# Optimization experiments

Measured on AMD Instinct MI355X. Metric: run time of the kernel, lower is better.

Reference implementation:

```python
import jax, jax.numpy as jnp
import numpy as np

EPS = 1e-5

def rmsnorm(x, w):
    return x * jax.lax.rsqrt(jnp.mean(x * x, axis=-1, keepdims=True) + EPS) * w

def setup_inputs() -> dict:
    key = jax.random.key(0)
    ks = jax.random.split(key, 10)
    b, d, n, k, r, l = 64, 256, 16, 4, 16, 256
    inp = {}
    inp['x_1'] = jax.random.normal(ks[0], (b, d), jnp.float32)
    inp['x_2'] = jax.random.normal(ks[1], (b, d), jnp.float32)
    inp['norm_w'] = jnp.ones((d,), jnp.float32)
    inp['conv_w'] = jax.random.normal(ks[2], (d, 1, k), jnp.float32) * 0.2
    inp['conv_b'] = jax.random.normal(ks[3], (d,), jnp.float32) * 0.02
    inp['in_w'] = jax.random.normal(ks[4], (2 * d, d), jnp.float32) * 0.02
    inp['xproj_w'] = jax.random.normal(ks[5], (r + 2 * n, d), jnp.float32) * 0.02
    inp['dt_w'] = jax.random.normal(ks[6], (d, r), jnp.float32) * 0.02
    inp['dt_b'] = jax.random.normal(ks[7], (d,), jnp.float32) * 0.02
    inp['out_w'] = jax.random.normal(ks[8], (d, d), jnp.float32) * 0.02
    # A = repeat(arange(1, n+1), 'n -> d n'); A_log = log(A)
    inp['A_log'] = jnp.tile(jnp.log(jnp.arange(1, n + 1, dtype=jnp.float32)), (d, 1))
    inp['D'] = jnp.ones((d,), jnp.float32)
    inp['l'] = l
    return inp

def _dwconv(x, conv_w, conv_b, l):
    # x: (b, l, d); depthwise causal-ish conv with padding k-1 on both sides, truncate to l
    d = x.shape[-1]
    k = conv_w.shape[-1]
    xt = x.transpose(0, 2, 1)  # (b, d, l)
    out = jax.lax.conv_general_dilated(
        xt, conv_w, window_strides=(1,), padding=[(k - 1, k - 1)],
        dimension_numbers=('NCH', 'OIH', 'NCH'), feature_group_count=d)
    out = out[:, :, :l] + conv_b[None, :, None]
    return out.transpose(0, 2, 1)  # (b, l, d)

def reference(x_1, x_2, norm_w, conv_w, conv_b, in_w, xproj_w, dt_w, dt_b, out_w, A_log, D, l):
    b, d = x_1.shape
    n = A_log.shape[1]
    r = dt_w.shape[1]
    # RMSNorm then broadcast along sequence
    x1 = jnp.broadcast_to(rmsnorm(x_1, norm_w)[:, None, :], (b, l, d))
    x2 = jnp.broadcast_to(rmsnorm(x_2, norm_w)[:, None, :], (b, l, d))
    # in_proj (no bias), split into x and res
    xr1 = x1 @ in_w.T
    x1c, res1 = xr1[..., :d], xr1[..., d:]
    xr2 = x2 @ in_w.T
    x2c, _ = xr2[..., :d], xr2[..., d:]
    # depthwise conv + silu
    x1s = jax.nn.silu(_dwconv(x1c, conv_w, conv_b, l))
    x2s = jax.nn.silu(_dwconv(x2c, conv_w, conv_b, l))
    # ssm: delta/B/C from x2s, scanned input u = x1s
    A = -jnp.exp(A_log)  # (d, n)
    xdbl = x2s @ xproj_w.T  # (b, l, r + 2n)
    delta, B, C = xdbl[..., :r], xdbl[..., r:r + n], xdbl[..., r + n:]
    delta = jax.nn.softplus(delta @ dt_w.T + dt_b)  # (b, l, d)
    deltaA = jnp.exp(jnp.einsum('bld,dn->bldn', delta, A))  # (b, l, d, n)
    dBu = (delta * x1s)[..., None] * B[:, :, None, :]  # (b, l, d, n)
    def step(h, inputs):
        dA_i, dBu_i, C_i = inputs  # (b,d,n), (b,d,n), (b,n)
        h = dA_i * h + dBu_i
        y = jnp.einsum('bdn,bn->bd', h, C_i)
        return h, y
    h0 = jnp.zeros((b, d, n), x1s.dtype)
    _, ys = jax.lax.scan(step, h0, (deltaA.transpose(1, 0, 2, 3),
                                     dBu.transpose(1, 0, 2, 3),
                                     C.transpose(1, 0, 2)))
    y = ys.transpose(1, 0, 2) + x1s * D  # (b, l, d)
    y = y * jax.nn.silu(res1)
    out = rmsnorm(y @ out_w.T, norm_w)
    return out[:, -1, :]
```

## Files before the change

### kernel.cpp

```cpp
#include <hip/hip_runtime.h>
#include <math.h>

#define D 256
#define N 16
#define R 16

#define WS_X1C  0
#define WS_RES1 16384
#define WS_X2C  32768

__device__ __forceinline__ float silu_f(float x) { return x / (1.0f + expf(-x)); }
__device__ __forceinline__ float softplus_f(float x) {
    return fmaxf(x, 0.0f) + log1pf(expf(-fabsf(x)));
}

__global__ __launch_bounds__(256) void k_inw(
    const float* __restrict__ x1_in, const float* __restrict__ x2_in,
    const float* __restrict__ norm_w, const float* __restrict__ in_w,
    float* __restrict__ ws)
{
    __shared__ float s_n[D];
    __shared__ float s_red[4];
    const int t  = threadIdx.x;
    const int g0 = blockIdx.x * 64;
    const int b  = g0 / 768;
    const int o0 = g0 % 768;
    const bool use2 = (o0 >= 512);
    const int q = t & 3;
    const int o = o0 + (t >> 2);
    const int row = (o >= 512) ? (o - 512) : o;

    const float* __restrict__ wr = in_w + (size_t)row * D;
    float4 w[16];
    #pragma unroll
    for (int k = 0; k < 16; ++k) w[k] = *(const float4*)(wr + q * 4 + 16 * k);

    const float* __restrict__ xrow = (use2 ? x2_in : x1_in) + (size_t)b * D;
    const float v = xrow[t];
    float p = v * v;
    #pragma unroll
    for (int off = 32; off >= 1; off >>= 1) p += __shfl_down(p, off, 64);
    if ((t & 63) == 0) s_red[t >> 6] = p;
    __syncthreads();
    const float ss = s_red[0] + s_red[1] + s_red[2] + s_red[3];
    s_n[t] = v * rsqrtf(ss * (1.0f / D) + 1e-5f) * norm_w[t];
    __syncthreads();

    float acc = 0.0f;
    #pragma unroll
    for (int k = 0; k < 16; ++k) {
        const int e = q * 4 + 16 * k;
        const float4 n4 = *(const float4*)(s_n + e);
        acc += w[k].x*n4.x + w[k].y*n4.y + w[k].z*n4.z + w[k].w*n4.w;
    }
    acc += __shfl_xor(acc, 1, 64);
    acc += __shfl_xor(acc, 2, 64);
    if (q == 0) {
        const int jj = o & 255;
        float* dst = (o < 256) ? (ws + WS_X1C)
                   : (o < 512) ? (ws + WS_RES1)
                               : (ws + WS_X2C);
        dst[b * D + jj] = acc;
    }
}

__global__ __launch_bounds__(1024) void k_fused(
    const float* __restrict__ conv_w, const float* __restrict__ conv_b,
    const float* __restrict__ xproj_w, const float* __restrict__ dt_w,
    const float* __restrict__ dt_b, const float* __restrict__ A_log,
    const float* __restrict__ Dp, const int* __restrict__ l_ptr,
    const float* __restrict__ out_w, const float* __restrict__ norm_w,
    const float* __restrict__ ws, float* __restrict__ out)
{
    __shared__ float s_x2s[4][D];
    __shared__ float s_xdbl[4][48];
    __shared__ float s_y[D];
    __shared__ float s_z[D];
    __shared__ float s_red[4];
    const int b = blockIdx.x;
    const int t = threadIdx.x;
    const int l = *l_ptr;
    const int q   = t & 3;
    const int dot = t >> 2;

    const float* __restrict__ orow = out_w + (size_t)dot * D;
    float4 wo[8];
    #pragma unroll
    for (int k = 0; k < 8; ++k) wo[k] = *(const float4*)(orow + q * 4 + 16 * k);

    float x1c = 0.0f, x2c = 0.0f, res1 = 0.0f, cb = 0.0f, dtb = 0.0f,
          dpj = 0.0f, wnj = 0.0f;
    float4 cw = make_float4(0.f, 0.f, 0.f, 0.f);
    float dtr[R];
    float alog[N];
    if (t < D) {
        x1c  = ws[WS_X1C  + b * D + t];
        x2c  = ws[WS_X2C  + b * D + t];
        res1 = ws[WS_RES1 + b * D + t];
        cw   = *(const float4*)(conv_w + 4 * t);
        cb   = conv_b[t];
        dtb  = dt_b[t];
        dpj  = Dp[t];
        wnj  = norm_w[t];
        const float* __restrict__ dtrow = dt_w + (size_t)t * R;
        #pragma unroll
        for (int qq = 0; qq < R; ++qq) dtr[qq] = dtrow[qq];
        const float* __restrict__ arow = A_log + (size_t)t * N;
        #pragma unroll
        for (int n = 0; n < N; ++n) alog[n] = arow[n];
    }

    float x1s[4];
    if (t < D) {
        float ksum[4];
        ksum[0] = cw.w;
        ksum[1] = cw.z + cw.w;
        ksum[2] = cw.y + cw.z + cw.w;
        ksum[3] = cw.x + cw.y + cw.z + cw.w;
        #pragma unroll
        for (int tc = 0; tc < 4; ++tc) {
            x1s[tc] = silu_f(ksum[tc] * x1c + cb);
            s_x2s[tc][t] = silu_f(ksum[tc] * x2c + cb);
        }
    }
    __syncthreads();

    if (t < 768) {
        const int tc = dot / 48;
        const int o  = dot % 48;
        const float* __restrict__ pr = xproj_w + (size_t)o * D;
        const float* __restrict__ xs = s_x2s[tc];
        float acc = 0.0f;
        #pragma unroll
        for (int k = 0; k < 16; ++k) {
            const int e = q * 4 + 16 * k;
            const float4 p4 = *(const float4*)(pr + e);
            const float4 x4 = *(const float4*)(xs + e);
            acc += p4.x*x4.x + p4.y*x4.y + p4.z*x4.z + p4.w*x4.w;
        }
        acc += __shfl_xor(acc, 1, 64);
        acc += __shfl_xor(acc, 2, 64);
        if (q == 0) s_xdbl[tc][o] = acc;
    }
    __syncthreads();

    if (t < D) {
        float delta[4];
        #pragma unroll
        for (int tc = 0; tc < 4; ++tc) {
            float acc = 0.0f;
            #pragma unroll
            for (int qq = 0; qq < R; ++qq) acc += s_xdbl[tc][qq] * dtr[qq];
            delta[tc] = softplus_f(acc + dtb);
        }
        float Aa[N];
        #pragma unroll
        for (int n = 0; n < N; ++n) Aa[n] = -expf(alog[n]);
        float h[N];
        #pragma unroll
        for (int n = 0; n < N; ++n) h[n] = 0.0f;
        const int nexp = (l < 3) ? l : 3;
        for (int tt = 0; tt < nexp; ++tt) {
            const float dl = delta[tt];
            const float du = dl * x1s[tt];
            #pragma unroll
            for (int n = 0; n < N; ++n) {
                const float dA = expf(dl * Aa[n]);
                h[n] = dA * h[n] + du * s_xdbl[tt][16 + n];
            }
        }
        if (l > 3) {
            const float dl = delta[3];
            const float du = dl * x1s[3];
            const float steps = (float)(l - 3);
            #pragma unroll
            for (int n = 0; n < N; ++n) {
                const float z   = dl * Aa[n];
                const float em1 = expm1f(z);
                const float emN = expm1f(steps * z);
                const float ratio = (em1 != 0.0f) ? (emN / em1) : steps;
                const float pw = emN + 1.0f;
                h[n] = pw * h[n] + du * s_xdbl[3][16 + n] * ratio;
            }
        }
        const int fc = ((l - 1) < 3) ? (l - 1) : 3;
        float y = 0.0f;
        #pragma unroll
        for (int n = 0; n < N; ++n) y += h[n] * s_xdbl[fc][32 + n];
        y += x1s[fc] * dpj;
        y *= silu_f(res1);
        s_y[t] = y;
    }
    __syncthreads();

    {
        float4 wo2[8];
        #pragma unroll
        for (int k = 0; k < 8; ++k)
            wo2[k] = *(const float4*)(orow + q * 4 + 16 * (8 + k));
        float acc = 0.0f;
        #pragma unroll
        for (int k = 0; k < 8; ++k) {
            const int e = q * 4 + 16 * k;
            const float4 y4 = *(const float4*)(s_y + e);
            acc += wo[k].x*y4.x + wo[k].y*y4.y + wo[k].z*y4.z + wo[k].w*y4.w;
        }
        #pragma unroll
        for (int k = 0; k < 8; ++k) {
            const int e = q * 4 + 16 * (8 + k);
            const float4 y4 = *(const float4*)(s_y + e);
            acc += wo2[k].x*y4.x + wo2[k].y*y4.y + wo2[k].z*y4.z + wo2[k].w*y4.w;
        }
        acc += __shfl_xor(acc, 1, 64);
        acc += __shfl_xor(acc, 2, 64);
        if (q == 0) s_z[dot] = acc;
    }
    __syncthreads();

    if (t < D) {
        const float zz = s_z[t];
        float p = zz * zz;
        #pragma unroll
        for (int off = 32; off >= 1; off >>= 1) p += __shfl_down(p, off, 64);
        if ((t & 63) == 0) s_red[t >> 6] = p;
    }
    __syncthreads();
    if (t < D) {
        const float ss = s_red[0] + s_red[1] + s_red[2] + s_red[3];
        out[b * D + t] = s_z[t] * rsqrtf(ss * (1.0f / D) + 1e-5f) * wnj;
    }
}

extern "C" void kernel_launch(void* const* d_in, const int* in_sizes, int n_in,
                              void* d_out, int out_size, void* d_ws, size_t ws_size,
                              hipStream_t stream) {
    const float* x1      = (const float*)d_in[0];
    const float* x2      = (const float*)d_in[1];
    const float* norm_w  = (const float*)d_in[2];
    const float* conv_w  = (const float*)d_in[3];
    const float* conv_b  = (const float*)d_in[4];
    const float* in_w    = (const float*)d_in[5];
    const float* xproj_w = (const float*)d_in[6];
    const float* dt_w    = (const float*)d_in[7];
    const float* dt_b    = (const float*)d_in[8];
    const float* out_w   = (const float*)d_in[9];
    const float* A_log   = (const float*)d_in[10];
    const float* Dp      = (const float*)d_in[11];
    const int*   l_ptr   = (const int*)d_in[12];
    float* out = (float*)d_out;
    float* ws  = (float*)d_ws;

    const int batch = in_sizes[0] / D;

    k_inw<<<dim3(batch * 12), dim3(256), 0, stream>>>(x1, x2, norm_w, in_w, ws);
    k_fused<<<dim3(batch), dim3(1024), 0, stream>>>(conv_w, conv_b, xproj_w,
                                                    dt_w, dt_b, A_log, Dp, l_ptr,
                                                    out_w, norm_w, ws, out);
}
```

Before: 94.24 us.

## Fuse in-projection and SSM kernels into one producer/consumer launch with spin flags

Merges the two launches into a single kernel. The first 3*batch blocks compute the RMSNorm plus in_proj slices and publish each slice with a release-flag token in the workspace. The remaining batch blocks load their weights, then spin on the three tokens for their batch before running the conv/SSM/out-proj path. This removes a kernel launch and the gap between kernels. In exchange it depends on all blocks being co-resident, and the tokens are never cleared, so on repeated calls consumers can read the workspace before the producers of that call have written it.

```diff
diff --git a/kernel.cpp b/kernel.cpp
--- a/kernel.cpp
+++ b/kernel.cpp
@@ -4,110 +4,137 @@
 #define D 256
 #define N 16
 #define R 16
+#define MAGIC 0x5A17C0DEu
 
 #define WS_X1C  0
 #define WS_RES1 16384
 #define WS_X2C  32768
+#define WS_TOK  49152
 
 __device__ __forceinline__ float silu_f(float x) { return x / (1.0f + expf(-x)); }
 __device__ __forceinline__ float softplus_f(float x) {
     return fmaxf(x, 0.0f) + log1pf(expf(-fabsf(x)));
 }
 
-__global__ __launch_bounds__(256) void k_inw(
+__global__ __launch_bounds__(1024) void k_mamba_pc(
     const float* __restrict__ x1_in, const float* __restrict__ x2_in,
-    const float* __restrict__ norm_w, const float* __restrict__ in_w,
-    float* __restrict__ ws)
+    const float* __restrict__ norm_w, const float* __restrict__ conv_w,
+    const float* __restrict__ conv_b, const float* __restrict__ in_w,
+    const float* __restrict__ xproj_w, const float* __restrict__ dt_w,
+    const float* __restrict__ dt_b, const float* __restrict__ out_w,
+    const float* __restrict__ A_log, const float* __restrict__ Dp,
+    const int* __restrict__ l_ptr, float* __restrict__ ws,
+    float* __restrict__ out, int nbatch)
 {
     __shared__ float s_n[D];
     __shared__ float s_red[4];
-    const int t  = threadIdx.x;
-    const int g0 = blockIdx.x * 64;
-    const int b  = g0 / 768;
-    const int o0 = g0 % 768;
-    const bool use2 = (o0 >= 512);
-    const int q = t & 3;
-    const int o = o0 + (t >> 2);
-    const int row = (o >= 512) ? (o - 512) : o;
-
-    const float* __restrict__ wr = in_w + (size_t)row * D;
-    float4 w[16];
-    #pragma unroll
-    for (int k = 0; k < 16; ++k) w[k] = *(const float4*)(wr + q * 4 + 16 * k);
-
-    const float* __restrict__ xrow = (use2 ? x2_in : x1_in) + (size_t)b * D;
-    const float v = xrow[t];
-    float p = v * v;
-    #pragma unroll
-    for (int off = 32; off >= 1; off >>= 1) p += __shfl_down(p, off, 64);
-    if ((t & 63) == 0) s_red[t >> 6] = p;
-    __syncthreads();
-    const float ss = s_red[0] + s_red[1] + s_red[2] + s_red[3];
-    s_n[t] = v * rsqrtf(ss * (1.0f / D) + 1e-5f) * norm_w[t];
-    __syncthreads();
-
-    float acc = 0.0f;
-    #pragma unroll
-    for (int k = 0; k < 16; ++k) {
-        const int e = q * 4 + 16 * k;
-        const float4 n4 = *(const float4*)(s_n + e);
-        acc += w[k].x*n4.x + w[k].y*n4.y + w[k].z*n4.z + w[k].w*n4.w;
-    }
-    acc += __shfl_xor(acc, 1, 64);
-    acc += __shfl_xor(acc, 2, 64);
-    if (q == 0) {
-        const int jj = o & 255;
-        float* dst = (o < 256) ? (ws + WS_X1C)
-                   : (o < 512) ? (ws + WS_RES1)
-                               : (ws + WS_X2C);
-        dst[b * D + jj] = acc;
-    }
-}
-
-__global__ __launch_bounds__(1024) void k_fused(
-    const float* __restrict__ conv_w, const float* __restrict__ conv_b,
-    const float* __restrict__ xproj_w, const float* __restrict__ dt_w,
-    const float* __restrict__ dt_b, const float* __restrict__ A_log,
-    const float* __restrict__ Dp, const int* __restrict__ l_ptr,
-    const float* __restrict__ out_w, const float* __restrict__ norm_w,
-    const float* __restrict__ ws, float* __restrict__ out)
-{
     __shared__ float s_x2s[4][D];
     __shared__ float s_xdbl[4][48];
     __shared__ float s_y[D];
     __shared__ float s_z[D];
-    __shared__ float s_red[4];
-    const int b = blockIdx.x;
-    const int t = threadIdx.x;
-    const int l = *l_ptr;
+
+    const int t   = threadIdx.x;
     const int q   = t & 3;
     const int dot = t >> 2;
+    const int nprod = nbatch * 3;
+    unsigned int* __restrict__ tok = (unsigned int*)(ws + WS_TOK);
+
+    if ((int)blockIdx.x < nprod) {
+        const int p = blockIdx.x;
+        const int b = p / 3;
+        const int c = p % 3;
+        const int row = (c == 1) ? (D + dot) : dot;
+
+        const float* __restrict__ wr = in_w + (size_t)row * D;
+        float4 w[16];
+        #pragma unroll
+        for (int k = 0; k < 16; ++k) w[k] = *(const float4*)(wr + q * 4 + 16 * k);
+
+        const float* __restrict__ xrow = ((c == 2) ? x2_in : x1_in) + (size_t)b * D;
+        float v = 0.0f;
+        if (t < D) {
+            v = xrow[t];
+            float pp = v * v;
+            #pragma unroll
+            for (int off = 32; off >= 1; off >>= 1) pp += __shfl_down(pp, off, 64);
+            if ((t & 63) == 0) s_red[t >> 6] = pp;
+        }
+        __syncthreads();
+        if (t < D) {
+            const float ss = s_red[0] + s_red[1] + s_red[2] + s_red[3];
+            s_n[t] = v * rsqrtf(ss * (1.0f / D) + 1e-5f) * norm_w[t];
+        }
+        __syncthreads();
+
+        float acc = 0.0f;
+        #pragma unroll
+        for (int k = 0; k < 16; ++k) {
+            const int e = q * 4 + 16 * k;
+            const float4 n4 = *(const float4*)(s_n + e);
+            acc += w[k].x*n4.x + w[k].y*n4.y + w[k].z*n4.z + w[k].w*n4.w;
+        }
+        acc += __shfl_xor(acc, 1, 64);
+        acc += __shfl_xor(acc, 2, 64);
+        if (q == 0) {
+            const int off = (c == 0) ? WS_X1C : (c == 1) ? WS_RES1 : WS_X2C;
+            __hip_atomic_exchange(&ws[off + b * D + dot], acc,
+                                  __ATOMIC_RELAXED, __HIP_MEMORY_SCOPE_AGENT);
+        }
+        __syncthreads();
+        if (t == 0)
+            __hip_atomic_exchange(&tok[p], MAGIC,
+                                  __ATOMIC_RELEASE, __HIP_MEMORY_SCOPE_AGENT);
+        return;
+    }
+
+    const int b = blockIdx.x - nprod;
+    const int l = *l_ptr;
 
     const float* __restrict__ orow = out_w + (size_t)dot * D;
     float4 wo[8];
     #pragma unroll
     for (int k = 0; k < 8; ++k) wo[k] = *(const float4*)(orow + q * 4 + 16 * k);
 
-    float x1c = 0.0f, x2c = 0.0f, res1 = 0.0f, cb = 0.0f, dtb = 0.0f,
-          dpj = 0.0f, wnj = 0.0f;
+    float cb = 0.0f, dtb = 0.0f, dpj = 0.0f, wnj = 0.0f;
     float4 cw = make_float4(0.f, 0.f, 0.f, 0.f);
     float dtr[R];
     float alog[N];
     if (t < D) {
-        x1c  = ws[WS_X1C  + b * D + t];
-        x2c  = ws[WS_X2C  + b * D + t];
-        res1 = ws[WS_RES1 + b * D + t];
-        cw   = *(const float4*)(conv_w + 4 * t);
-        cb   = conv_b[t];
-        dtb  = dt_b[t];
-        dpj  = Dp[t];
-        wnj  = norm_w[t];
+        cw  = *(const float4*)(conv_w + 4 * t);
+        cb  = conv_b[t];
+        dtb = dt_b[t];
+        dpj = Dp[t];
+        wnj = norm_w[t];
         const float* __restrict__ dtrow = dt_w + (size_t)t * R;
         #pragma unroll
         for (int qq = 0; qq < R; ++qq) dtr[qq] = dtrow[qq];
         const float* __restrict__ arow = A_log + (size_t)t * N;
         #pragma unroll
         for (int n = 0; n < N; ++n) alog[n] = arow[n];
+    }
+
+    if (t == 0) {
+        #pragma unroll
+        for (int s = 0; s < 3; ++s) {
+            int spin = 0;
+            while (__hip_atomic_load(&tok[3 * b + s], __ATOMIC_ACQUIRE,
+                                     __HIP_MEMORY_SCOPE_AGENT) != MAGIC &&
+                   spin < (1 << 22)) {
+                ++spin;
+                __builtin_amdgcn_s_sleep(2);
+            }
+        }
+    }
+    __syncthreads();
+
+    float x1c = 0.0f, x2c = 0.0f, res1 = 0.0f;
+    if (t < D) {
+        x1c  = __hip_atomic_load(&ws[WS_X1C  + b * D + t], __ATOMIC_RELAXED,
+                                 __HIP_MEMORY_SCOPE_AGENT);
+        x2c  = __hip_atomic_load(&ws[WS_X2C  + b * D + t], __ATOMIC_RELAXED,
+                                 __HIP_MEMORY_SCOPE_AGENT);
+        res1 = __hip_atomic_load(&ws[WS_RES1 + b * D + t], __ATOMIC_RELAXED,
+                                 __HIP_MEMORY_SCOPE_AGENT);
     }
 
     float x1s[4];
@@ -252,8 +279,7 @@
 
     const int batch = in_sizes[0] / D;
 
-    k_inw<<<dim3(batch * 12), dim3(256), 0, stream>>>(x1, x2, norm_w, in_w, ws);
-    k_fused<<<dim3(batch), dim3(1024), 0, stream>>>(conv_w, conv_b, xproj_w,
-                                                    dt_w, dt_b, A_log, Dp, l_ptr,
-                                                    out_w, norm_w, ws, out);
+    k_mamba_pc<<<dim3(batch * 4), dim3(1024), 0, stream>>>(
+        x1, x2, norm_w, conv_w, conv_b, in_w, xproj_w, dt_w, dt_b,
+        out_w, A_log, Dp, l_ptr, ws, out, batch);
 }
```

Result: slower. 98.72 us (+4.8%).

## Move conv and xproj projection into first kernel, split per batch into three blocks

Applied to the files above, without the earlier changes.

The first kernel now runs 1024-thread blocks, three per batch row (x1c, res1, x2c). The x2c block also applies the conv and silu and computes the xproj dot products, writing xdbl to workspace. The second kernel then only loads the precomputed xdbl and skips one barrier phase and the xproj weight reads. This moves work off the serialized per-batch tail kernel and spreads it over more blocks. The cost is larger first-kernel blocks, where only a third of the blocks do the extra phase, so the load is unbalanced.

```diff
diff --git a/kernel.cpp b/kernel.cpp
--- a/kernel.cpp
+++ b/kernel.cpp
@@ -7,43 +7,52 @@
 
 #define WS_X1C  0
 #define WS_RES1 16384
-#define WS_X2C  32768
+#define WS_XDBL 32768
 
 __device__ __forceinline__ float silu_f(float x) { return x / (1.0f + expf(-x)); }
 __device__ __forceinline__ float softplus_f(float x) {
     return fmaxf(x, 0.0f) + log1pf(expf(-fabsf(x)));
 }
 
-__global__ __launch_bounds__(256) void k_inw(
+__global__ __launch_bounds__(1024) void k1_produce(
     const float* __restrict__ x1_in, const float* __restrict__ x2_in,
-    const float* __restrict__ norm_w, const float* __restrict__ in_w,
-    float* __restrict__ ws)
+    const float* __restrict__ norm_w, const float* __restrict__ conv_w,
+    const float* __restrict__ conv_b, const float* __restrict__ in_w,
+    const float* __restrict__ xproj_w, float* __restrict__ ws)
 {
     __shared__ float s_n[D];
     __shared__ float s_red[4];
-    const int t  = threadIdx.x;
-    const int g0 = blockIdx.x * 64;
-    const int b  = g0 / 768;
-    const int o0 = g0 % 768;
-    const bool use2 = (o0 >= 512);
-    const int q = t & 3;
-    const int o = o0 + (t >> 2);
-    const int row = (o >= 512) ? (o - 512) : o;
+    __shared__ float s_x2s[4][D];
+    const int t   = threadIdx.x;
+    const int q   = t & 3;
+    const int dot = t >> 2;
+    const int b   = blockIdx.x / 3;
+    const int c   = blockIdx.x % 3;
+    const int row = (c == 1) ? (D + dot) : dot;
 
     const float* __restrict__ wr = in_w + (size_t)row * D;
     float4 w[16];
     #pragma unroll
     for (int k = 0; k < 16; ++k) w[k] = *(const float4*)(wr + q * 4 + 16 * k);
 
-    const float* __restrict__ xrow = (use2 ? x2_in : x1_in) + (size_t)b * D;
-    const float v = xrow[t];
-    float p = v * v;
-    #pragma unroll
-    for (int off = 32; off >= 1; off >>= 1) p += __shfl_down(p, off, 64);
-    if ((t & 63) == 0) s_red[t >> 6] = p;
-    __syncthreads();
-    const float ss = s_red[0] + s_red[1] + s_red[2] + s_red[3];
-    s_n[t] = v * rsqrtf(ss * (1.0f / D) + 1e-5f) * norm_w[t];
+    float4 cw = make_float4(0.f, 0.f, 0.f, 0.f);
+    float cb = 0.0f;
+    if (c == 2 && t < D) { cw = *(const float4*)(conv_w + 4 * t); cb = conv_b[t]; }
+
+    const float* __restrict__ xrow = ((c == 2) ? x2_in : x1_in) + (size_t)b * D;
+    float v = 0.0f;
+    if (t < D) {
+        v = xrow[t];
+        float pp = v * v;
+        #pragma unroll
+        for (int off = 32; off >= 1; off >>= 1) pp += __shfl_down(pp, off, 64);
+        if ((t & 63) == 0) s_red[t >> 6] = pp;
+    }
+    __syncthreads();
+    if (t < D) {
+        const float ss = s_red[0] + s_red[1] + s_red[2] + s_red[3];
+        s_n[t] = v * rsqrtf(ss * (1.0f / D) + 1e-5f) * norm_w[t];
+    }
     __syncthreads();
 
     float acc = 0.0f;
@@ -55,47 +64,83 @@
     }
     acc += __shfl_xor(acc, 1, 64);
     acc += __shfl_xor(acc, 2, 64);
-    if (q == 0) {
-        const int jj = o & 255;
-        float* dst = (o < 256) ? (ws + WS_X1C)
-                   : (o < 512) ? (ws + WS_RES1)
-                               : (ws + WS_X2C);
-        dst[b * D + jj] = acc;
-    }
-}
-
-__global__ __launch_bounds__(1024) void k_fused(
+
+    if (c == 0) {
+        if (q == 0) ws[WS_X1C + b * D + dot] = acc;
+        return;
+    }
+    if (c == 1) {
+        if (q == 0) ws[WS_RES1 + b * D + dot] = acc;
+        return;
+    }
+
+    if (q == 0) s_n[dot] = acc;
+    __syncthreads();
+    if (t < D) {
+        const float x2c = s_n[t];
+        float ksum[4];
+        ksum[0] = cw.w;
+        ksum[1] = cw.z + cw.w;
+        ksum[2] = cw.y + cw.z + cw.w;
+        ksum[3] = cw.x + cw.y + cw.z + cw.w;
+        #pragma unroll
+        for (int tc = 0; tc < 4; ++tc)
+            s_x2s[tc][t] = silu_f(ksum[tc] * x2c + cb);
+    }
+    __syncthreads();
+
+    if (t < 768) {
+        const int tc = dot / 48;
+        const int o  = dot % 48;
+        const float* __restrict__ pr = xproj_w + (size_t)o * D;
+        const float* __restrict__ xs = s_x2s[tc];
+        float a2 = 0.0f;
+        #pragma unroll
+        for (int k = 0; k < 16; ++k) {
+            const int e = q * 4 + 16 * k;
+            const float4 p4 = *(const float4*)(pr + e);
+            const float4 x4 = *(const float4*)(xs + e);
+            a2 += p4.x*x4.x + p4.y*x4.y + p4.z*x4.z + p4.w*x4.w;
+        }
+        a2 += __shfl_xor(a2, 1, 64);
+        a2 += __shfl_xor(a2, 2, 64);
+        if (q == 0) ws[WS_XDBL + b * 192 + tc * 48 + o] = a2;
+    }
+}
+
+__global__ __launch_bounds__(1024) void k2_consume(
     const float* __restrict__ conv_w, const float* __restrict__ conv_b,
-    const float* __restrict__ xproj_w, const float* __restrict__ dt_w,
-    const float* __restrict__ dt_b, const float* __restrict__ A_log,
-    const float* __restrict__ Dp, const int* __restrict__ l_ptr,
-    const float* __restrict__ out_w, const float* __restrict__ norm_w,
-    const float* __restrict__ ws, float* __restrict__ out)
+    const float* __restrict__ dt_w, const float* __restrict__ dt_b,
+    const float* __restrict__ A_log, const float* __restrict__ Dp,
+    const int* __restrict__ l_ptr, const float* __restrict__ out_w,
+    const float* __restrict__ norm_w, const float* __restrict__ ws,
+    float* __restrict__ out)
 {
-    __shared__ float s_x2s[4][D];
-    __shared__ float s_xdbl[4][48];
+    __shared__ float s_xdbl[192];
     __shared__ float s_y[D];
     __shared__ float s_z[D];
     __shared__ float s_red[4];
     const int b = blockIdx.x;
     const int t = threadIdx.x;
-    const int l = *l_ptr;
     const int q   = t & 3;
     const int dot = t >> 2;
+    const int l = *l_ptr;
 
     const float* __restrict__ orow = out_w + (size_t)dot * D;
     float4 wo[8];
     #pragma unroll
     for (int k = 0; k < 8; ++k) wo[k] = *(const float4*)(orow + q * 4 + 16 * k);
 
-    float x1c = 0.0f, x2c = 0.0f, res1 = 0.0f, cb = 0.0f, dtb = 0.0f,
-          dpj = 0.0f, wnj = 0.0f;
+    float xd = 0.0f;
+    if (t < 192) xd = ws[WS_XDBL + b * 192 + t];
+
+    float x1c = 0.0f, res1 = 0.0f, cb = 0.0f, dtb = 0.0f, dpj = 0.0f,
+          wnj = 0.0f;
     float4 cw = make_float4(0.f, 0.f, 0.f, 0.f);
     float dtr[R];
     float alog[N];
     if (t < D) {
         x1c  = ws[WS_X1C  + b * D + t];
-        x2c  = ws[WS_X2C  + b * D + t];
         res1 = ws[WS_RES1 + b * D + t];
         cw   = *(const float4*)(conv_w + 4 * t);
         cb   = conv_b[t];
@@ -109,48 +154,22 @@
         #pragma unroll
         for (int n = 0; n < N; ++n) alog[n] = arow[n];
     }
-
-    float x1s[4];
+    if (t < 192) s_xdbl[t] = xd;
+    __syncthreads();
+
     if (t < D) {
         float ksum[4];
         ksum[0] = cw.w;
         ksum[1] = cw.z + cw.w;
         ksum[2] = cw.y + cw.z + cw.w;
         ksum[3] = cw.x + cw.y + cw.z + cw.w;
+        float x1s[4], delta[4];
         #pragma unroll
         for (int tc = 0; tc < 4; ++tc) {
             x1s[tc] = silu_f(ksum[tc] * x1c + cb);
-            s_x2s[tc][t] = silu_f(ksum[tc] * x2c + cb);
-        }
-    }
-    __syncthreads();
-
-    if (t < 768) {
-        const int tc = dot / 48;
-        const int o  = dot % 48;
-        const float* __restrict__ pr = xproj_w + (size_t)o * D;
-        const float* __restrict__ xs = s_x2s[tc];
-        float acc = 0.0f;
-        #pragma unroll
-        for (int k = 0; k < 16; ++k) {
-            const int e = q * 4 + 16 * k;
-            const float4 p4 = *(const float4*)(pr + e);
-            const float4 x4 = *(const float4*)(xs + e);
-            acc += p4.x*x4.x + p4.y*x4.y + p4.z*x4.z + p4.w*x4.w;
-        }
-        acc += __shfl_xor(acc, 1, 64);
-        acc += __shfl_xor(acc, 2, 64);
-        if (q == 0) s_xdbl[tc][o] = acc;
-    }
-    __syncthreads();
-
-    if (t < D) {
-        float delta[4];
-        #pragma unroll
-        for (int tc = 0; tc < 4; ++tc) {
             float acc = 0.0f;
             #pragma unroll
-            for (int qq = 0; qq < R; ++qq) acc += s_xdbl[tc][qq] * dtr[qq];
+            for (int qq = 0; qq < R; ++qq) acc += s_xdbl[tc * 48 + qq] * dtr[qq];
             delta[tc] = softplus_f(acc + dtb);
         }
         float Aa[N];
@@ -166,7 +185,7 @@
             #pragma unroll
             for (int n = 0; n < N; ++n) {
                 const float dA = expf(dl * Aa[n]);
-                h[n] = dA * h[n] + du * s_xdbl[tt][16 + n];
+                h[n] = dA * h[n] + du * s_xdbl[tt * 48 + 16 + n];
             }
         }
         if (l > 3) {
@@ -180,13 +199,13 @@
                 const float emN = expm1f(steps * z);
                 const float ratio = (em1 != 0.0f) ? (emN / em1) : steps;
                 const float pw = emN + 1.0f;
-                h[n] = pw * h[n] + du * s_xdbl[3][16 + n] * ratio;
+                h[n] = pw * h[n] + du * s_xdbl[3 * 48 + 16 + n] * ratio;
             }
         }
         const int fc = ((l - 1) < 3) ? (l - 1) : 3;
         float y = 0.0f;
         #pragma unroll
-        for (int n = 0; n < N; ++n) y += h[n] * s_xdbl[fc][32 + n];
+        for (int n = 0; n < N; ++n) y += h[n] * s_xdbl[fc * 48 + 32 + n];
         y += x1s[fc] * dpj;
         y *= silu_f(res1);
         s_y[t] = y;
@@ -252,8 +271,8 @@
 
     const int batch = in_sizes[0] / D;
 
-    k_inw<<<dim3(batch * 12), dim3(256), 0, stream>>>(x1, x2, norm_w, in_w, ws);
-    k_fused<<<dim3(batch), dim3(1024), 0, stream>>>(conv_w, conv_b, xproj_w,
-                                                    dt_w, dt_b, A_log, Dp, l_ptr,
-                                                    out_w, norm_w, ws, out);
-}
+    k1_produce<<<dim3(batch * 3), dim3(1024), 0, stream>>>(
+        x1, x2, norm_w, conv_w, conv_b, in_w, xproj_w, ws);
+    k2_consume<<<dim3(batch), dim3(1024), 0, stream>>>(
+        conv_w, conv_b, dt_w, dt_b, A_log, Dp, l_ptr, out_w, norm_w, ws, out);
+}
```

Result: no change. 92.98 us (-1.3%).

## Share in_w rows across x1/x2 projections and reuse xproj weights across conv taps

Applied to the files above, without the earlier changes.

The in_proj kernel now launches 4 blocks of 1024 threads per batch row. Each block loads a 128-row slice of in_w once and computes both the x1 and x2 projections for the first 512 outputs, so the separate x2 pass that reread the same weights is gone. In the fused kernel, the xproj weights are preloaded into registers before the first barrier, and each thread now computes all four conv-tap dot products from the same weights, with a 16-lane reduction in place of a 4-lane one. The out_w preload is also moved after the other parameter loads. Bigger blocks and more live registers may reduce occupancy.

```diff
diff --git a/kernel.cpp b/kernel.cpp
--- a/kernel.cpp
+++ b/kernel.cpp
@@ -14,57 +14,77 @@
     return fmaxf(x, 0.0f) + log1pf(expf(-fabsf(x)));
 }
 
-__global__ __launch_bounds__(256) void k_inw(
+__global__ __launch_bounds__(1024) void k1_inw(
     const float* __restrict__ x1_in, const float* __restrict__ x2_in,
     const float* __restrict__ norm_w, const float* __restrict__ in_w,
     float* __restrict__ ws)
 {
-    __shared__ float s_n[D];
-    __shared__ float s_red[4];
+    __shared__ float s_n1[D];
+    __shared__ float s_n2[D];
+    __shared__ float s_red[8];
     const int t  = threadIdx.x;
-    const int g0 = blockIdx.x * 64;
-    const int b  = g0 / 768;
-    const int o0 = g0 % 768;
-    const bool use2 = (o0 >= 512);
-    const int q = t & 3;
-    const int o = o0 + (t >> 2);
-    const int row = (o >= 512) ? (o - 512) : o;
+    const int b  = blockIdx.x >> 2;
+    const int cc = blockIdx.x & 3;
+    const int q8 = t & 7;
+    const int r8 = t >> 3;
+    const int row = cc * 128 + r8;
+    const bool dual = (cc < 2);
 
     const float* __restrict__ wr = in_w + (size_t)row * D;
-    float4 w[16];
+    float4 w[8];
     #pragma unroll
-    for (int k = 0; k < 16; ++k) w[k] = *(const float4*)(wr + q * 4 + 16 * k);
-
-    const float* __restrict__ xrow = (use2 ? x2_in : x1_in) + (size_t)b * D;
-    const float v = xrow[t];
-    float p = v * v;
+    for (int k = 0; k < 8; ++k) w[k] = *(const float4*)(wr + 4 * q8 + 32 * k);
+
+    float v1 = 0.0f, v2 = 0.0f;
+    if (t < D) {
+        v1 = x1_in[b * D + t];
+        float p1 = v1 * v1, p2 = 0.0f;
+        if (dual) { v2 = x2_in[b * D + t]; p2 = v2 * v2; }
+        #pragma unroll
+        for (int off = 32; off >= 1; off >>= 1) {
+            p1 += __shfl_down(p1, off, 64);
+            p2 += __shfl_down(p2, off, 64);
+        }
+        if ((t & 63) == 0) { s_red[t >> 6] = p1; s_red[4 + (t >> 6)] = p2; }
+    }
+    __syncthreads();
+    if (t < D) {
+        const float ss1 = s_red[0] + s_red[1] + s_red[2] + s_red[3];
+        const float wn = norm_w[t];
+        s_n1[t] = v1 * rsqrtf(ss1 * (1.0f / D) + 1e-5f) * wn;
+        if (dual) {
+            const float ss2 = s_red[4] + s_red[5] + s_red[6] + s_red[7];
+            s_n2[t] = v2 * rsqrtf(ss2 * (1.0f / D) + 1e-5f) * wn;
+        }
+    }
+    __syncthreads();
+
+    float a1 = 0.0f, a2 = 0.0f;
     #pragma unroll
-    for (int off = 32; off >= 1; off >>= 1) p += __shfl_down(p, off, 64);
-    if ((t & 63) == 0) s_red[t >> 6] = p;
-    __syncthreads();
-    const float ss = s_red[0] + s_red[1] + s_red[2] + s_red[3];
-    s_n[t] = v * rsqrtf(ss * (1.0f / D) + 1e-5f) * norm_w[t];
-    __syncthreads();
-
-    float acc = 0.0f;
-    #pragma unroll
-    for (int k = 0; k < 16; ++k) {
-        const int e = q * 4 + 16 * k;
-        const float4 n4 = *(const float4*)(s_n + e);
-        acc += w[k].x*n4.x + w[k].y*n4.y + w[k].z*n4.z + w[k].w*n4.w;
-    }
-    acc += __shfl_xor(acc, 1, 64);
-    acc += __shfl_xor(acc, 2, 64);
-    if (q == 0) {
-        const int jj = o & 255;
-        float* dst = (o < 256) ? (ws + WS_X1C)
-                   : (o < 512) ? (ws + WS_RES1)
-                               : (ws + WS_X2C);
-        dst[b * D + jj] = acc;
-    }
-}
-
-__global__ __launch_bounds__(1024) void k_fused(
+    for (int k = 0; k < 8; ++k) {
+        const int e = 4 * q8 + 32 * k;
+        const float4 n4 = *(const float4*)(s_n1 + e);
+        a1 += w[k].x*n4.x + w[k].y*n4.y + w[k].z*n4.z + w[k].w*n4.w;
+        if (dual) {
+            const float4 m4 = *(const float4*)(s_n2 + e);
+            a2 += w[k].x*m4.x + w[k].y*m4.y + w[k].z*m4.z + w[k].w*m4.w;
+        }
+    }
+    a1 += __shfl_xor(a1, 1, 64); a1 += __shfl_xor(a1, 2, 64); a1 += __shfl_xor(a1, 4, 64);
+    if (dual) {
+        a2 += __shfl_xor(a2, 1, 64); a2 += __shfl_xor(a2, 2, 64); a2 += __shfl_xor(a2, 4, 64);
+    }
+    if (q8 == 0) {
+        if (dual) {
+            ws[WS_X1C + b * D + row] = a1;
+            ws[WS_X2C + b * D + row] = a2;
+        } else {
+            ws[WS_RES1 + b * D + (row - 256)] = a1;
+        }
+    }
+}
+
+__global__ __launch_bounds__(1024) void k2_rest(
     const float* __restrict__ conv_w, const float* __restrict__ conv_b,
     const float* __restrict__ xproj_w, const float* __restrict__ dt_w,
     const float* __restrict__ dt_b, const float* __restrict__ A_log,
@@ -73,20 +93,15 @@
     const float* __restrict__ ws, float* __restrict__ out)
 {
     __shared__ float s_x2s[4][D];
-    __shared__ float s_xdbl[4][48];
+    __shared__ float s_xdbl[192];
     __shared__ float s_y[D];
     __shared__ float s_z[D];
     __shared__ float s_red[4];
     const int b = blockIdx.x;
     const int t = threadIdx.x;
-    const int l = *l_ptr;
     const int q   = t & 3;
     const int dot = t >> 2;
-
-    const float* __restrict__ orow = out_w + (size_t)dot * D;
-    float4 wo[8];
-    #pragma unroll
-    for (int k = 0; k < 8; ++k) wo[k] = *(const float4*)(orow + q * 4 + 16 * k);
+    const int l = *l_ptr;
 
     float x1c = 0.0f, x2c = 0.0f, res1 = 0.0f, cb = 0.0f, dtb = 0.0f,
           dpj = 0.0f, wnj = 0.0f;
@@ -109,6 +124,18 @@
         #pragma unroll
         for (int n = 0; n < N; ++n) alog[n] = arow[n];
     }
+    const int xo = t >> 4;
+    const int xs = t & 15;
+    float4 wx[4];
+    if (t < 768) {
+        const float* __restrict__ pr = xproj_w + (size_t)xo * D;
+        #pragma unroll
+        for (int k = 0; k < 4; ++k) wx[k] = *(const float4*)(pr + 4 * xs + 64 * k);
+    }
+    const float* __restrict__ orow = out_w + (size_t)dot * D;
+    float4 wo[8];
+    #pragma unroll
+    for (int k = 0; k < 8; ++k) wo[k] = *(const float4*)(orow + q * 4 + 16 * k);
 
     float x1s[4];
     if (t < D) {
@@ -126,21 +153,27 @@
     __syncthreads();
 
     if (t < 768) {
-        const int tc = dot / 48;
-        const int o  = dot % 48;
-        const float* __restrict__ pr = xproj_w + (size_t)o * D;
-        const float* __restrict__ xs = s_x2s[tc];
-        float acc = 0.0f;
-        #pragma unroll
-        for (int k = 0; k < 16; ++k) {
-            const int e = q * 4 + 16 * k;
-            const float4 p4 = *(const float4*)(pr + e);
-            const float4 x4 = *(const float4*)(xs + e);
-            acc += p4.x*x4.x + p4.y*x4.y + p4.z*x4.z + p4.w*x4.w;
-        }
-        acc += __shfl_xor(acc, 1, 64);
-        acc += __shfl_xor(acc, 2, 64);
-        if (q == 0) s_xdbl[tc][o] = acc;
+        float acc[4] = {0.f, 0.f, 0.f, 0.f};
+        #pragma unroll
+        for (int k = 0; k < 4; ++k) {
+            const int e = 4 * xs + 64 * k;
+            #pragma unroll
+            for (int tc = 0; tc < 4; ++tc) {
+                const float4 x4 = *(const float4*)(&s_x2s[tc][e]);
+                acc[tc] += wx[k].x*x4.x + wx[k].y*x4.y + wx[k].z*x4.z + wx[k].w*x4.w;
+            }
+        }
+        #pragma unroll
+        for (int tc = 0; tc < 4; ++tc) {
+            acc[tc] += __shfl_xor(acc[tc], 1, 64);
+            acc[tc] += __shfl_xor(acc[tc], 2, 64);
+            acc[tc] += __shfl_xor(acc[tc], 4, 64);
+            acc[tc] += __shfl_xor(acc[tc], 8, 64);
+        }
+        if (xs == 0) {
+            #pragma unroll
+            for (int tc = 0; tc < 4; ++tc) s_xdbl[tc * 48 + xo] = acc[tc];
+        }
     }
     __syncthreads();
 
@@ -150,7 +183,7 @@
         for (int tc = 0; tc < 4; ++tc) {
             float acc = 0.0f;
             #pragma unroll
-            for (int qq = 0; qq < R; ++qq) acc += s_xdbl[tc][qq] * dtr[qq];
+            for (int qq = 0; qq < R; ++qq) acc += s_xdbl[tc * 48 + qq] * dtr[qq];
             delta[tc] = softplus_f(acc + dtb);
         }
         float Aa[N];
@@ -166,7 +199,7 @@
             #pragma unroll
             for (int n = 0; n < N; ++n) {
                 const float dA = expf(dl * Aa[n]);
-                h[n] = dA * h[n] + du * s_xdbl[tt][16 + n];
+                h[n] = dA * h[n] + du * s_xdbl[tt * 48 + 16 + n];
             }
         }
         if (l > 3) {
@@ -180,13 +213,13 @@
                 const float emN = expm1f(steps * z);
                 const float ratio = (em1 != 0.0f) ? (emN / em1) : steps;
                 const float pw = emN + 1.0f;
-                h[n] = pw * h[n] + du * s_xdbl[3][16 + n] * ratio;
+                h[n] = pw * h[n] + du * s_xdbl[3 * 48 + 16 + n] * ratio;
             }
         }
         const int fc = ((l - 1) < 3) ? (l - 1) : 3;
         float y = 0.0f;
         #pragma unroll
-        for (int n = 0; n < N; ++n) y += h[n] * s_xdbl[fc][32 + n];
+        for (int n = 0; n < N; ++n) y += h[n] * s_xdbl[fc * 48 + 32 + n];
         y += x1s[fc] * dpj;
         y *= silu_f(res1);
         s_y[t] = y;
@@ -252,8 +285,8 @@
 
     const int batch = in_sizes[0] / D;
 
-    k_inw<<<dim3(batch * 12), dim3(256), 0, stream>>>(x1, x2, norm_w, in_w, ws);
-    k_fused<<<dim3(batch), dim3(1024), 0, stream>>>(conv_w, conv_b, xproj_w,
+    k1_inw<<<dim3(batch * 4), dim3(1024), 0, stream>>>(x1, x2, norm_w, in_w, ws);
+    k2_rest<<<dim3(batch), dim3(1024), 0, stream>>>(conv_w, conv_b, xproj_w,
                                                     dt_w, dt_b, A_log, Dp, l_ptr,
                                                     out_w, norm_w, ws, out);
 }
```

New measurement: 92.30 us. 1.02x faster.
